# Kernel optimization log

Measured on AMD Instinct MI355X. Metric: run time of the kernel, lower is better.

## Reference

```python
import jax, jax.numpy as jnp
import numpy as np

D_MODEL = 1024
NUM_HEADS = 16
D_K = D_MODEL // NUM_HEADS


def setup_inputs() -> dict:
    key = jax.random.key(0)
    k1, k2, k3, k4 = jax.random.split(key, 4)
    scale = 1.0 / np.sqrt(D_MODEL)
    inp = {
        "input": jax.random.normal(k1, (2, 2048, D_MODEL), dtype=jnp.float32),
        "W_qkv": jax.random.normal(k2, (D_MODEL, 3 * D_MODEL), dtype=jnp.float32) * scale,
        "b_qkv": jax.random.normal(k3, (3 * D_MODEL,), dtype=jnp.float32) * 0.02,
        "W_out": jax.random.normal(k4, (D_MODEL, D_MODEL), dtype=jnp.float32) * scale,
    }
    return inp


def reference(input, W_qkv, b_qkv, W_out):
    B, S, _ = input.shape
    qkv = input @ W_qkv + b_qkv                      # [B,S,3D]
    q, k, v = jnp.split(qkv, 3, axis=-1)             # each [B,S,D]
    def heads(x):
        return x.reshape(B, S, NUM_HEADS, D_K).transpose(0, 2, 1, 3)  # [B,H,S,dk]
    q, k, v = heads(q), heads(k), heads(v)
    scores = jnp.einsum("bhsd,bhtd->bhst", q, k) / jnp.sqrt(jnp.float32(D_K))
    attn = jax.nn.softmax(scores, axis=-1)           # [B,H,S,S]
    out = jnp.einsum("bhst,bhtd->bhsd", attn, v)     # [B,H,S,dk]
    out = out.transpose(0, 2, 1, 3).reshape(B, S, D_MODEL)
    return out @ W_out
```

## Files before the change

### kernel.cpp

```cpp
#include <hip/hip_runtime.h>

typedef unsigned short u16;
typedef unsigned int u32;
typedef __attribute__((ext_vector_type(8))) short short8;
typedef __attribute__((ext_vector_type(8))) __bf16 bf16x8;
typedef __attribute__((ext_vector_type(4))) float f32x4;
typedef __attribute__((ext_vector_type(16))) float f32x16;

__device__ __forceinline__ u16 f2bf(float f) {
  union { float f; u32 u; } c; c.f = f;
  u32 u = c.u + 0x7fffu + ((c.u >> 16) & 1u);
  return (u16)(u >> 16);
}
__device__ __forceinline__ f32x4 mfma16(short8 a, short8 b, f32x4 c) {
  return __builtin_amdgcn_mfma_f32_16x16x32_bf16(
      __builtin_bit_cast(bf16x8, a), __builtin_bit_cast(bf16x8, b), c, 0, 0, 0);
}
__device__ __forceinline__ f32x16 mfma32(short8 a, short8 b, f32x16 c) {
  return __builtin_amdgcn_mfma_f32_32x32x16_bf16(
      __builtin_bit_cast(bf16x8, a), __builtin_bit_cast(bf16x8, b), c, 0, 0, 0);
}
__device__ __forceinline__ float fexp2(float x) {
  float r; asm("v_exp_f32 %0, %1" : "=v"(r) : "v"(x)); return r;
}
__device__ __forceinline__ void gl16(const u16* g, u16* l) {
  __builtin_amdgcn_global_load_lds(
      (const __attribute__((address_space(1))) unsigned*)g,
      (__attribute__((address_space(3))) unsigned*)l, 16, 0, 0);
}


__global__ __launch_bounds__(256) void transpose_f32_bf16(const float* __restrict__ in,
                                                          u16* __restrict__ out,
                                                          int R, int C) {
  __shared__ u16 tile[32][33];
  int tx = threadIdx.x & 31, ty = threadIdx.x >> 5;
  int c0 = blockIdx.x * 32, r0 = blockIdx.y * 32;
  for (int i = 0; i < 32; i += 8)
    tile[ty + i][tx] = f2bf(in[(size_t)(r0 + ty + i) * C + c0 + tx]);
  __syncthreads();
  for (int i = 0; i < 32; i += 8)
    out[(size_t)(c0 + ty + i) * R + r0 + tx] = tile[tx][ty + i];
}

template <int MODE, int BM>
__global__ __launch_bounds__(256) void gemm_bt(const void* __restrict__ Av,
                                               const void* __restrict__ Bv,
                                               const float* __restrict__ bias,
                                               void* __restrict__ C0v,
                                               void* __restrict__ C1v,
                                               int M, int N, int K) {
  constexpr int MI  = BM / 32;
  constexpr int NSA = BM / 8;
  constexpr int ASZ = (MODE == 1) ? 9216 : NSA * 512;
  constexpr int BSZ = (MODE == 2) ? 9216 : 8192;
  __shared__ __align__(16) u16 As[2][ASZ];
  __shared__ __align__(16) u16 Bs[2][BSZ];
  const int tid = threadIdx.x;
  const int w = tid >> 6, l = tid & 63;
  const int i16 = l & 15, q4 = l >> 4;

  const int nbx = gridDim.x;
  const int nwg = nbx * gridDim.y;
  int fid = blockIdx.y * nbx + blockIdx.x;
  int wg = (nwg & 7) ? fid : ((fid & 7) * (nwg >> 3) + (fid >> 3));
  const int m0 = (wg / nbx) * BM, n0 = (wg % nbx) * 128;
  const int wm = (w >> 1) * (BM / 2), wn = (w & 1) * 64;

  const int arow = tid >> 3, akg = (tid & 7) * 8;

  const u16* A16p = (const u16*)Av;
  const u16* B16p = (const u16*)Bv;
  const float* Fp = (MODE == 1) ? (const float*)Av : (const float*)Bv;
  const int fbase = (MODE == 1) ? m0 : n0;

  f32x4 acc[MI][4] = {};
  float4 pf[4][2];

#define STAGE_A16(bufi, kk) {                                                  \
    _Pragma("unroll") for (int i = 0; i < NSA / 4; ++i) {                      \
      const int s = w * (NSA / 4) + i;                                         \
      gl16(&A16p[(size_t)(m0 + (s >> 1) * 16 + i16) * K + (kk) + (s & 1) * 32  \
                 + q4 * 8],                                                    \
           &As[bufi][s * 512]); } }
#define STAGE_B16(bufi, kk) {                                                  \
    _Pragma("unroll") for (int i = 0; i < 4; ++i) {                            \
      const int s = w * 4 + i;                                                 \
      gl16(&B16p[(size_t)(n0 + (s >> 1) * 16 + i16) * K + (kk) + (s & 1) * 32  \
                 + q4 * 8],                                                    \
           &Bs[bufi][s * 512]); } }
#define LOAD_PFX(kk) {                                                         \
    _Pragma("unroll") for (int i = 0; i < 4; ++i) {                            \
      const float* src = Fp + (size_t)(fbase + arow + i * 32) * K + (kk) + akg;\
      pf[i][0] = *(const float4*)src;                                          \
      pf[i][1] = *(const float4*)(src + 4); } }
#define CVT_X(bufi) {                                                          \
    _Pragma("unroll") for (int i = 0; i < 4; ++i) {                            \
      short8 v;                                                                \
      v[0] = (short)f2bf(pf[i][0].x); v[1] = (short)f2bf(pf[i][0].y);          \
      v[2] = (short)f2bf(pf[i][0].z); v[3] = (short)f2bf(pf[i][0].w);          \
      v[4] = (short)f2bf(pf[i][1].x); v[5] = (short)f2bf(pf[i][1].y);          \
      v[6] = (short)f2bf(pf[i][1].z); v[7] = (short)f2bf(pf[i][1].w);          \
      u16* d = (MODE == 1) ? &As[bufi][(arow + i * 32) * 72 + akg]             \
                           : &Bs[bufi][(arow + i * 32) * 72 + akg];            \
      *(short8*)d = v; } }

  const int nk = K >> 6;
  if constexpr (MODE == 0) {
    STAGE_A16(0, 0); STAGE_B16(0, 0);
  } else if constexpr (MODE == 1) {
    LOAD_PFX(0); STAGE_B16(0, 0); CVT_X(0); LOAD_PFX(64);
  } else {
    LOAD_PFX(0); STAGE_A16(0, 0); CVT_X(0); LOAD_PFX(64);
  }
  __syncthreads();

  for (int t = 0; t < nk; ++t) {
    const int cur = t & 1, nxt = cur ^ 1;
    const int k1 = (t + 1) << 6;
    if (t + 1 < nk) {
      if constexpr (MODE == 0) {
        STAGE_A16(nxt, k1); STAGE_B16(nxt, k1);
      } else if constexpr (MODE == 1) {
        STAGE_B16(nxt, k1); CVT_X(nxt);
        if (t + 2 < nk) LOAD_PFX(k1 + 64);
      } else {
        STAGE_A16(nxt, k1); CVT_X(nxt);
        if (t + 2 < nk) LOAD_PFX(k1 + 64);
      }
    }
#pragma unroll
    for (int ks = 0; ks < 2; ++ks) {
      short8 af[MI], bfr[4];
#pragma unroll
      for (int mi = 0; mi < MI; ++mi) {
        if constexpr (MODE == 1)
          af[mi] = *(short8*)&As[cur][(wm + mi * 16 + i16) * 72 + ks * 32 + q4 * 8];
        else
          af[mi] = *(short8*)((char*)&As[cur][0] +
                              (((wm >> 4) + mi) * 2 + ks) * 1024 + l * 16);
      }
#pragma unroll
      for (int ni = 0; ni < 4; ++ni) {
        if constexpr (MODE == 2)
          bfr[ni] = *(short8*)&Bs[cur][(wn + ni * 16 + i16) * 72 + ks * 32 + q4 * 8];
        else
          bfr[ni] = *(short8*)((char*)&Bs[cur][0] +
                               (((wn >> 4) + ni) * 2 + ks) * 1024 + l * 16);
      }
#pragma unroll
      for (int mi = 0; mi < MI; ++mi)
#pragma unroll
        for (int ni = 0; ni < 4; ++ni)
          acc[mi][ni] = mfma16(af[mi], bfr[ni], acc[mi][ni]);
    }
    __syncthreads();
  }
#undef STAGE_A16
#undef STAGE_B16
#undef LOAD_PFX
#undef CVT_X

  if constexpr (MODE == 0) {
    float* dstf = (float*)C0v;
    for (int mi = 0; mi < MI; ++mi) {
      int row = m0 + wm + mi * 16 + q4 * 4;
      for (int ni = 0; ni < 4; ++ni) {
        int nl = wn + ni * 16 + i16;
        for (int r = 0; r < 4; ++r)
          dstf[(size_t)(row + r) * N + n0 + nl] = acc[mi][ni][r];
      }
    }
  } else if constexpr (MODE == 1) {
    if (n0 < 1024) {
      u16* dstb = (u16*)C0v;
      for (int mi = 0; mi < MI; ++mi) {
        int row = m0 + wm + mi * 16 + q4 * 4;
        for (int ni = 0; ni < 4; ++ni) {
          int nl = wn + ni * 16 + i16;
          float b = bias[n0 + nl];
          for (int r = 0; r < 4; ++r)
            dstb[(size_t)(row + r) * 1024 + n0 + nl] = f2bf(acc[mi][ni][r] + b);
        }
      }
    } else {
      u16* KT = (u16*)C1v;
      for (int mi = 0; mi < MI; ++mi) {
        int row = m0 + wm + mi * 16 + q4 * 4;
        for (int ni = 0; ni < 4; ++ni) {
          int nl = wn + ni * 16 + i16;
          const int d = (n0 - 1024) + nl;
          const int hh = d >> 6, dh = d & 63;
          const int sd = (dh >> 4) << 1;
          const int lh = ((dh >> 3) & 1) << 5;
          const int j = dh & 7;
          float b = bias[n0 + nl];
          for (int r = 0; r < 4; ++r) {
            const int tok = row + r;
            const int bb = tok >> 11, t = tok & 2047;
            size_t addr = ((size_t)((bb << 4) + hh) * 32 + (t >> 6)) * 4096
                        + (sd + ((t >> 5) & 1)) * 512 + (lh + (t & 31)) * 8 + j;
            KT[addr] = f2bf(acc[mi][ni][r] + b);
          }
        }
      }
    }
  } else {
    u16* VTt = (u16*)C0v;
    for (int mi = 0; mi < MI; ++mi) {
      int drow = m0 + wm + mi * 16 + q4 * 4;
      float4 bv = *(const float4*)&bias[drow];
      const float bvr[4] = {bv.x, bv.y, bv.z, bv.w};
      for (int ni = 0; ni < 4; ++ni) {
        int col = n0 + wn + ni * 16 + i16;
        const int bb = col >> 11, t = col & 2047;
        const int su = ((t >> 4) & 3) << 1;
        const int lt = ((t >> 3) & 1) << 5;
        const int j = t & 7;
        const size_t tb0 = ((size_t)(bb << 4) * 32 + (t >> 6)) * 4096;
        for (int r = 0; r < 4; ++r) {
          const int d = drow + r;
          const int hh = d >> 6, dh = d & 63;
          size_t addr = tb0 + (size_t)hh * 131072
                      + (su + (dh >> 5)) * 512 + (lt + (dh & 31)) * 8 + j;
          VTt[addr] = f2bf(acc[mi][ni][r] + bvr[r]);
        }
      }
    }
  }
}

__global__ __launch_bounds__(512, 4) void attn_flash(u16* __restrict__ Qbuf,
                                                     const u16* __restrict__ Kall,
                                                     const u16* __restrict__ VTall) {
  constexpr float CSC = 0.18033688011112042f;
  constexpr float MC  = 96.0f * CSC;
  __shared__ __align__(16) u16 SH[32768];
  __shared__ float RsumB[128], RsumT[128];

  const int tid = threadIdx.x;
  const int w = tid >> 6, l = tid & 63;
  const int l31 = l & 31, hi = l >> 5;
  const int qg = w >> 1, th = w & 1;

  u16* KsL = SH + th * 16384;
  u16* VsL = SH + th * 16384 + 8192;

  const int L = blockIdx.x;
  const int xcd = L & 7, rr = L >> 3;
  const int qb = rr & 15, gg = rr >> 4;
  const int g = gg * 8 + xcd;
  const int h = g & 15, bat = g >> 4;
  const int q0 = qb * 128;

  u16* Q = Qbuf + (size_t)bat * 2048 * 1024;
  const u16* ksrc = Kall + (size_t)((bat << 4) + h) * 131072 + l * 8;
  const u16* vsrc = VTall + (size_t)((bat << 4) + h) * 131072 + l * 8;

  short8 qf[4];
  {
    const u16* qrow = Q + (size_t)(q0 + qg * 32 + l31) * 1024 + h * 64 + hi * 8;
#pragma unroll
    for (int ks = 0; ks < 4; ++ks) qf[ks] = *(const short8*)(qrow + ks * 16);
  }

#define STAGE(buf_, it_) {                                                   \
    const size_t toff = (size_t)(it_) * 4096;                                \
    gl16(ksrc + toff + qg * 512,       KsL + (buf_) * 4096 + qg * 512);      \
    gl16(ksrc + toff + (qg + 4) * 512, KsL + (buf_) * 4096 + (qg + 4) * 512);\
    gl16(vsrc + toff + qg * 512,       VsL + (buf_) * 4096 + qg * 512);      \
    gl16(vsrc + toff + (qg + 4) * 512, VsL + (buf_) * 4096 + (qg + 4) * 512); }

  f32x16 o0 = {}, o1 = {};
  float sm0 = 0.f, sm1 = 0.f, sm2 = 0.f, sm3 = 0.f;

  const int tbase = th * 16;
  STAGE(0, tbase);
  __syncthreads();

  for (int i = 0; i < 16; ++i) {
    const int cur = i & 1;
    if (i + 1 < 16) STAGE(cur ^ 1, tbase + i + 1);

    const char* Kc = (const char*)KsL + cur * 8192 + l * 16;
    const char* Vc = (const char*)VsL + cur * 8192 + l * 16;

    f32x16 st0 = {}, st1 = {};
#pragma unroll
    for (int ks = 0; ks < 4; ++ks) {
      short8 kf0 = *(const short8*)(Kc + ks * 2048);
      short8 kf1 = *(const short8*)(Kc + ks * 2048 + 1024);
      st0 = mfma32(kf0, qf[ks], st0);
      st1 = mfma32(kf1, qf[ks], st1);
    }

    u32 W[16];
#define SOFTMAX_PACK(stt, WB) {                                             \
      float p_[16];                                                         \
      _Pragma("unroll") for (int r = 0; r < 16; ++r)                        \
          p_[r] = fexp2(__builtin_fmaf(stt[r], CSC, -MC));                  \
      _Pragma("unroll") for (int r = 0; r < 16; r += 4) {                   \
        sm0 += p_[r]; sm1 += p_[r + 1]; sm2 += p_[r + 2]; sm3 += p_[r + 3]; \
      }                                                                     \
      _Pragma("unroll") for (int m = 0; m < 4; ++m)                         \
        _Pragma("unroll") for (int s = 0; s < 2; ++s)                       \
          asm("v_cvt_pk_bf16_f32 %0, %1, %2"                                \
              : "=v"(W[(WB) + m * 2 + s])                                   \
              : "v"(p_[4 * m + 2 * s]), "v"(p_[4 * m + 2 * s + 1]));        \
    }
    SOFTMAX_PACK(st0, 0)
    SOFTMAX_PACK(st1, 8)
#undef SOFTMAX_PACK

#pragma unroll
    for (int u = 0; u < 4; ++u) {
      const int base = (u >> 1) * 8 + (u & 1) * 4;
      u32 a0 = W[base], a1 = W[base + 1], b0 = W[base + 2], b1 = W[base + 3];
      asm("v_permlane32_swap_b32 %0, %1" : "+v"(a0), "+v"(b0));
      asm("v_permlane32_swap_b32 %0, %1" : "+v"(a1), "+v"(b1));
      int4 af4;
      af4.x = (int)a0; af4.y = (int)a1; af4.z = (int)b0; af4.w = (int)b1;
      const short8 pfr = __builtin_bit_cast(short8, af4);
      const short8 vf0 = *(const short8*)(Vc + u * 2048);
      const short8 vf1 = *(const short8*)(Vc + u * 2048 + 1024);
      o0 = mfma32(pfr, vf0, o0);
      o1 = mfma32(pfr, vf1, o1);
    }
    __syncthreads();
  }
#undef STAGE

  float rs = (sm0 + sm1) + (sm2 + sm3);
  rs += __shfl_xor(rs, 32);
  __syncthreads();
  float* MF = (float*)SH;
  if (th == 1) {
    float* dst = MF + (qg * 64 + l) * 36;
    *(f32x16*)dst = o0;
    *(f32x16*)(dst + 16) = o1;
    if (hi == 0) RsumB[qg * 32 + l31] = rs;
  }
  __syncthreads();
  if (th == 0) {
    const float* src = MF + (qg * 64 + l) * 36;
    o0 += *(const f32x16*)src;
    o1 += *(const f32x16*)(src + 16);
    float rtot = rs + RsumB[qg * 32 + l31];
    if (hi == 0) RsumT[qg * 32 + l31] = rtot;
  }
  __syncthreads();
  if (th == 0) {
#pragma unroll
    for (int r = 0; r < 16; ++r) {
      const int qq = (r & 3) + 8 * (r >> 2) + 4 * hi;
      const float inv = 1.0f / RsumT[qg * 32 + qq];
      u16* dst = Q + (size_t)(q0 + qg * 32 + qq) * 1024 + h * 64 + l31;
      dst[0]  = f2bf(o0[r] * inv);
      dst[32] = f2bf(o1[r] * inv);
    }
  }
}

extern "C" void kernel_launch(void* const* d_in, const int* in_sizes, int n_in,
                              void* d_out, int out_size, void* d_ws, size_t ws_size,
                              hipStream_t stream) {
  const float* X    = (const float*)d_in[0];
  const float* Wqkv = (const float*)d_in[1];
  const float* bqkv = (const float*)d_in[2];
  const float* Wout = (const float*)d_in[3];

  u16* Qbuf = (u16*)d_out;
  u16* WT1  = Qbuf + (size_t)4096 * 1024;
  u16* WT2  = WT1 + (size_t)3072 * 1024;
  u16* Kbuf = (u16*)d_ws;
  u16* VT   = Kbuf + (size_t)4096 * 1024;
  float* Cws = (float*)d_ws;

  transpose_f32_bf16<<<dim3(96, 32), 256, 0, stream>>>(Wqkv, WT1, 1024, 3072);
  transpose_f32_bf16<<<dim3(32, 32), 256, 0, stream>>>(Wout, WT2, 1024, 1024);

  gemm_bt<1, 128><<<dim3(16, 32), 256, 0, stream>>>(
      X, WT1, bqkv, Qbuf, Kbuf, 4096, 2048, 1024);

  gemm_bt<2, 64><<<dim3(32, 16), 256, 0, stream>>>(
      WT1 + (size_t)2048 * 1024, X, bqkv + 2048, VT, nullptr, 1024, 4096, 1024);

  attn_flash<<<dim3(512), 512, 0, stream>>>(Qbuf, Kbuf, VT);

  gemm_bt<0, 64><<<dim3(8, 64), 256, 0, stream>>>(
      Qbuf, WT2, nullptr, Cws, nullptr, 4096, 1024, 1024);

  hipMemcpyAsync(d_out, Cws, (size_t)4096 * 1024 * sizeof(float),
                 hipMemcpyDeviceToDevice, stream);
}
```

Before: 218.8 us.

## Pre-convert X to bf16, retile QK projection GEMM, add MFMA priority hints

Adds a standalone kernel that converts the fp32 input X to bf16 once. The Q/K projection GEMM can then stage both operands with direct global-to-LDS bf16 loads instead of converting fp32 in registers, and it is retiled from BM=128 to BM=64 with twice as many workgroups. The attention kernel wraps its two MFMA phases in s_setprio raises so the matrix work gets issue priority over the softmax phase of other waves. The workspace is reorganized so the bf16 X buffer is later overwritten by V^T. The cost is an extra launch plus an extra pass over X in memory.

```diff
diff --git a/kernel.cpp b/kernel.cpp
--- a/kernel.cpp
+++ b/kernel.cpp
@@ -41,6 +41,19 @@
   __syncthreads();
   for (int i = 0; i < 32; i += 8)
     out[(size_t)(c0 + ty + i) * R + r0 + tx] = tile[tx][ty + i];
+}
+
+__global__ __launch_bounds__(256) void f32_to_bf16(const float* __restrict__ in,
+                                                   u16* __restrict__ out) {
+  const size_t base = ((size_t)blockIdx.x * 256 + threadIdx.x) * 8;
+  float4 f0 = *(const float4*)(in + base);
+  float4 f1 = *(const float4*)(in + base + 4);
+  short8 v;
+  v[0] = (short)f2bf(f0.x); v[1] = (short)f2bf(f0.y);
+  v[2] = (short)f2bf(f0.z); v[3] = (short)f2bf(f0.w);
+  v[4] = (short)f2bf(f1.x); v[5] = (short)f2bf(f1.y);
+  v[6] = (short)f2bf(f1.z); v[7] = (short)f2bf(f1.w);
+  *(short8*)&out[base] = v;
 }
 
 template <int MODE, int BM>
@@ -52,7 +65,7 @@
                                                int M, int N, int K) {
   constexpr int MI  = BM / 32;
   constexpr int NSA = BM / 8;
-  constexpr int ASZ = (MODE == 1) ? 9216 : NSA * 512;
+  constexpr int ASZ = NSA * 512;
   constexpr int BSZ = (MODE == 2) ? 9216 : 8192;
   __shared__ __align__(16) u16 As[2][ASZ];
   __shared__ __align__(16) u16 Bs[2][BSZ];
@@ -71,8 +84,8 @@
 
   const u16* A16p = (const u16*)Av;
   const u16* B16p = (const u16*)Bv;
-  const float* Fp = (MODE == 1) ? (const float*)Av : (const float*)Bv;
-  const int fbase = (MODE == 1) ? m0 : n0;
+  const float* Fp = (const float*)Bv;
+  const int fbase = n0;
 
   f32x4 acc[MI][4] = {};
   float4 pf[4][2];
@@ -101,17 +114,13 @@
       v[2] = (short)f2bf(pf[i][0].z); v[3] = (short)f2bf(pf[i][0].w);          \
       v[4] = (short)f2bf(pf[i][1].x); v[5] = (short)f2bf(pf[i][1].y);          \
       v[6] = (short)f2bf(pf[i][1].z); v[7] = (short)f2bf(pf[i][1].w);          \
-      u16* d = (MODE == 1) ? &As[bufi][(arow + i * 32) * 72 + akg]             \
-                           : &Bs[bufi][(arow + i * 32) * 72 + akg];            \
-      *(short8*)d = v; } }
+      *(short8*)&Bs[bufi][(arow + i * 32) * 72 + akg] = v; } }
 
   const int nk = K >> 6;
-  if constexpr (MODE == 0) {
+  if constexpr (MODE == 2) {
+    LOAD_PFX(0); STAGE_A16(0, 0); CVT_X(0); LOAD_PFX(64);
+  } else {
     STAGE_A16(0, 0); STAGE_B16(0, 0);
-  } else if constexpr (MODE == 1) {
-    LOAD_PFX(0); STAGE_B16(0, 0); CVT_X(0); LOAD_PFX(64);
-  } else {
-    LOAD_PFX(0); STAGE_A16(0, 0); CVT_X(0); LOAD_PFX(64);
   }
   __syncthreads();
 
@@ -119,27 +128,20 @@
     const int cur = t & 1, nxt = cur ^ 1;
     const int k1 = (t + 1) << 6;
     if (t + 1 < nk) {
-      if constexpr (MODE == 0) {
-        STAGE_A16(nxt, k1); STAGE_B16(nxt, k1);
-      } else if constexpr (MODE == 1) {
-        STAGE_B16(nxt, k1); CVT_X(nxt);
+      if constexpr (MODE == 2) {
+        STAGE_A16(nxt, k1); CVT_X(nxt);
         if (t + 2 < nk) LOAD_PFX(k1 + 64);
       } else {
-        STAGE_A16(nxt, k1); CVT_X(nxt);
-        if (t + 2 < nk) LOAD_PFX(k1 + 64);
+        STAGE_A16(nxt, k1); STAGE_B16(nxt, k1);
       }
     }
 #pragma unroll
     for (int ks = 0; ks < 2; ++ks) {
       short8 af[MI], bfr[4];
 #pragma unroll
-      for (int mi = 0; mi < MI; ++mi) {
-        if constexpr (MODE == 1)
-          af[mi] = *(short8*)&As[cur][(wm + mi * 16 + i16) * 72 + ks * 32 + q4 * 8];
-        else
-          af[mi] = *(short8*)((char*)&As[cur][0] +
-                              (((wm >> 4) + mi) * 2 + ks) * 1024 + l * 16);
-      }
+      for (int mi = 0; mi < MI; ++mi)
+        af[mi] = *(short8*)((char*)&As[cur][0] +
+                            (((wm >> 4) + mi) * 2 + ks) * 1024 + l * 16);
 #pragma unroll
       for (int ni = 0; ni < 4; ++ni) {
         if constexpr (MODE == 2)
@@ -286,6 +288,7 @@
     const char* Vc = (const char*)VsL + cur * 8192 + l * 16;
 
     f32x16 st0 = {}, st1 = {};
+    __builtin_amdgcn_s_setprio(1);
 #pragma unroll
     for (int ks = 0; ks < 4; ++ks) {
       short8 kf0 = *(const short8*)(Kc + ks * 2048);
@@ -293,6 +296,7 @@
       st0 = mfma32(kf0, qf[ks], st0);
       st1 = mfma32(kf1, qf[ks], st1);
     }
+    __builtin_amdgcn_s_setprio(0);
 
     u32 W[16];
 #define SOFTMAX_PACK(stt, WB) {                                             \
@@ -312,6 +316,7 @@
     SOFTMAX_PACK(st1, 8)
 #undef SOFTMAX_PACK
 
+    __builtin_amdgcn_s_setprio(1);
 #pragma unroll
     for (int u = 0; u < 4; ++u) {
       const int base = (u >> 1) * 8 + (u & 1) * 4;
@@ -326,6 +331,7 @@
       o0 = mfma32(pfr, vf0, o0);
       o1 = mfma32(pfr, vf1, o1);
     }
+    __builtin_amdgcn_s_setprio(0);
     __syncthreads();
   }
 #undef STAGE
@@ -372,20 +378,22 @@
   u16* Qbuf = (u16*)d_out;
   u16* WT1  = Qbuf + (size_t)4096 * 1024;
   u16* WT2  = WT1 + (size_t)3072 * 1024;
-  u16* Kbuf = (u16*)d_ws;
-  u16* VT   = Kbuf + (size_t)4096 * 1024;
+  u16* Xbf  = (u16*)d_ws;
+  u16* Kt   = (u16*)d_ws + (size_t)4096 * 1024;
+  u16* VTt  = (u16*)d_ws;
   float* Cws = (float*)d_ws;
 
   transpose_f32_bf16<<<dim3(96, 32), 256, 0, stream>>>(Wqkv, WT1, 1024, 3072);
   transpose_f32_bf16<<<dim3(32, 32), 256, 0, stream>>>(Wout, WT2, 1024, 1024);
-
-  gemm_bt<1, 128><<<dim3(16, 32), 256, 0, stream>>>(
-      X, WT1, bqkv, Qbuf, Kbuf, 4096, 2048, 1024);
+  f32_to_bf16<<<dim3(2048), 256, 0, stream>>>(X, Xbf);
+
+  gemm_bt<1, 64><<<dim3(16, 64), 256, 0, stream>>>(
+      Xbf, WT1, bqkv, Qbuf, Kt, 4096, 2048, 1024);
 
   gemm_bt<2, 64><<<dim3(32, 16), 256, 0, stream>>>(
-      WT1 + (size_t)2048 * 1024, X, bqkv + 2048, VT, nullptr, 1024, 4096, 1024);
-
-  attn_flash<<<dim3(512), 512, 0, stream>>>(Qbuf, Kbuf, VT);
+      WT1 + (size_t)2048 * 1024, X, bqkv + 2048, VTt, nullptr, 1024, 4096, 1024);
+
+  attn_flash<<<dim3(512), 512, 0, stream>>>(Qbuf, Kt, VTt);
 
   gemm_bt<0, 64><<<dim3(8, 64), 256, 0, stream>>>(
       Qbuf, WT2, nullptr, Cws, nullptr, 4096, 1024, 1024);
```

After: 245.1 us. 1.12x slower.

## Fuse Q/K/V projections into one GEMM with MFMA-tiled Q and output layout

Applied to the files above, without the earlier changes.

Merges the separate QKV GEMM (Q,K) and transposed V GEMM into a single launch over N=3072, with the V epilogue scattering into the tiled V layout directly. Q and the attention output are stored in a pre-swizzled 64x64 tile layout, so attention and the output-projection GEMM can load fragments contiguously (gl16 of whole tiles). This also removes the second pass that re-read and re-converted X to bf16. Adds s_setprio around MFMA blocks in attention. The epilogue scatter stores become more irregular, which may cost write efficiency.

```diff
diff --git a/kernel.cpp b/kernel.cpp
--- a/kernel.cpp
+++ b/kernel.cpp
@@ -45,17 +45,17 @@
 
 template <int MODE, int BM>
 __global__ __launch_bounds__(256) void gemm_bt(const void* __restrict__ Av,
-                                               const void* __restrict__ Bv,
+                                               const u16* __restrict__ Bv,
                                                const float* __restrict__ bias,
                                                void* __restrict__ C0v,
                                                void* __restrict__ C1v,
+                                               void* __restrict__ C2v,
                                                int M, int N, int K) {
   constexpr int MI  = BM / 32;
   constexpr int NSA = BM / 8;
   constexpr int ASZ = (MODE == 1) ? 9216 : NSA * 512;
-  constexpr int BSZ = (MODE == 2) ? 9216 : 8192;
   __shared__ __align__(16) u16 As[2][ASZ];
-  __shared__ __align__(16) u16 Bs[2][BSZ];
+  __shared__ __align__(16) u16 Bs[2][8192];
   const int tid = threadIdx.x;
   const int w = tid >> 6, l = tid & 63;
   const int i16 = l & 15, q4 = l >> 4;
@@ -70,28 +70,25 @@
   const int arow = tid >> 3, akg = (tid & 7) * 8;
 
   const u16* A16p = (const u16*)Av;
-  const u16* B16p = (const u16*)Bv;
-  const float* Fp = (MODE == 1) ? (const float*)Av : (const float*)Bv;
-  const int fbase = (MODE == 1) ? m0 : n0;
-
+  const float* Fp = (const float*)Av;
   f32x4 acc[MI][4] = {};
   float4 pf[4][2];
 
 #define STAGE_A16(bufi, kk) {                                                  \
     _Pragma("unroll") for (int i = 0; i < NSA / 4; ++i) {                      \
       const int s = w * (NSA / 4) + i;                                         \
-      gl16(&A16p[(size_t)(m0 + (s >> 1) * 16 + i16) * K + (kk) + (s & 1) * 32  \
-                 + q4 * 8],                                                    \
+      gl16(&A16p[((size_t)((m0 >> 6) * 16 + ((kk) >> 6))) * 4096 + s * 512     \
+                 + l * 8],                                                     \
            &As[bufi][s * 512]); } }
 #define STAGE_B16(bufi, kk) {                                                  \
     _Pragma("unroll") for (int i = 0; i < 4; ++i) {                            \
       const int s = w * 4 + i;                                                 \
-      gl16(&B16p[(size_t)(n0 + (s >> 1) * 16 + i16) * K + (kk) + (s & 1) * 32  \
-                 + q4 * 8],                                                    \
+      gl16(&Bv[(size_t)(n0 + (s >> 1) * 16 + i16) * K + (kk) + (s & 1) * 32    \
+               + q4 * 8],                                                      \
            &Bs[bufi][s * 512]); } }
 #define LOAD_PFX(kk) {                                                         \
     _Pragma("unroll") for (int i = 0; i < 4; ++i) {                            \
-      const float* src = Fp + (size_t)(fbase + arow + i * 32) * K + (kk) + akg;\
+      const float* src = Fp + (size_t)(m0 + arow + i * 32) * K + (kk) + akg;   \
       pf[i][0] = *(const float4*)src;                                          \
       pf[i][1] = *(const float4*)(src + 4); } }
 #define CVT_X(bufi) {                                                          \
@@ -101,17 +98,13 @@
       v[2] = (short)f2bf(pf[i][0].z); v[3] = (short)f2bf(pf[i][0].w);          \
       v[4] = (short)f2bf(pf[i][1].x); v[5] = (short)f2bf(pf[i][1].y);          \
       v[6] = (short)f2bf(pf[i][1].z); v[7] = (short)f2bf(pf[i][1].w);          \
-      u16* d = (MODE == 1) ? &As[bufi][(arow + i * 32) * 72 + akg]             \
-                           : &Bs[bufi][(arow + i * 32) * 72 + akg];            \
-      *(short8*)d = v; } }
+      *(short8*)&As[bufi][(arow + i * 32) * 72 + akg] = v; } }
 
   const int nk = K >> 6;
-  if constexpr (MODE == 0) {
-    STAGE_A16(0, 0); STAGE_B16(0, 0);
-  } else if constexpr (MODE == 1) {
+  if constexpr (MODE == 1) {
     LOAD_PFX(0); STAGE_B16(0, 0); CVT_X(0); LOAD_PFX(64);
   } else {
-    LOAD_PFX(0); STAGE_A16(0, 0); CVT_X(0); LOAD_PFX(64);
+    STAGE_A16(0, 0); STAGE_B16(0, 0);
   }
   __syncthreads();
 
@@ -119,14 +112,11 @@
     const int cur = t & 1, nxt = cur ^ 1;
     const int k1 = (t + 1) << 6;
     if (t + 1 < nk) {
-      if constexpr (MODE == 0) {
-        STAGE_A16(nxt, k1); STAGE_B16(nxt, k1);
-      } else if constexpr (MODE == 1) {
+      if constexpr (MODE == 1) {
         STAGE_B16(nxt, k1); CVT_X(nxt);
         if (t + 2 < nk) LOAD_PFX(k1 + 64);
       } else {
-        STAGE_A16(nxt, k1); CVT_X(nxt);
-        if (t + 2 < nk) LOAD_PFX(k1 + 64);
+        STAGE_A16(nxt, k1); STAGE_B16(nxt, k1);
       }
     }
 #pragma unroll
@@ -141,13 +131,9 @@
                               (((wm >> 4) + mi) * 2 + ks) * 1024 + l * 16);
       }
 #pragma unroll
-      for (int ni = 0; ni < 4; ++ni) {
-        if constexpr (MODE == 2)
-          bfr[ni] = *(short8*)&Bs[cur][(wn + ni * 16 + i16) * 72 + ks * 32 + q4 * 8];
-        else
-          bfr[ni] = *(short8*)((char*)&Bs[cur][0] +
-                               (((wn >> 4) + ni) * 2 + ks) * 1024 + l * 16);
-      }
+      for (int ni = 0; ni < 4; ++ni)
+        bfr[ni] = *(short8*)((char*)&Bs[cur][0] +
+                             (((wn >> 4) + ni) * 2 + ks) * 1024 + l * 16);
 #pragma unroll
       for (int mi = 0; mi < MI; ++mi)
 #pragma unroll
@@ -171,30 +157,31 @@
           dstf[(size_t)(row + r) * N + n0 + nl] = acc[mi][ni][r];
       }
     }
-  } else if constexpr (MODE == 1) {
-    if (n0 < 1024) {
-      u16* dstb = (u16*)C0v;
-      for (int mi = 0; mi < MI; ++mi) {
-        int row = m0 + wm + mi * 16 + q4 * 4;
-        for (int ni = 0; ni < 4; ++ni) {
-          int nl = wn + ni * 16 + i16;
-          float b = bias[n0 + nl];
-          for (int r = 0; r < 4; ++r)
-            dstb[(size_t)(row + r) * 1024 + n0 + nl] = f2bf(acc[mi][ni][r] + b);
-        }
-      }
-    } else {
-      u16* KT = (u16*)C1v;
-      for (int mi = 0; mi < MI; ++mi) {
-        int row = m0 + wm + mi * 16 + q4 * 4;
-        for (int ni = 0; ni < 4; ++ni) {
-          int nl = wn + ni * 16 + i16;
+  } else {
+    for (int mi = 0; mi < MI; ++mi) {
+      int row = m0 + wm + mi * 16 + q4 * 4;
+      for (int ni = 0; ni < 4; ++ni) {
+        int nl = wn + ni * 16 + i16;
+        float b = bias[n0 + nl];
+        if (n0 < 1024) {
+          u16* Qt = (u16*)C0v;
+          const int d = n0 + nl;
+          const int dt = d >> 6, dh = d & 63;
+          const int sc = (dh >> 5), sl = (((dh & 31) >> 3) << 4), j = dh & 7;
+          for (int r = 0; r < 4; ++r) {
+            const int tok = row + r;
+            size_t addr = ((size_t)((tok >> 6) * 16 + dt)) * 4096
+                        + ((((tok & 63) >> 4) << 1) + sc) * 512
+                        + ((tok & 15) + sl) * 8 + j;
+            Qt[addr] = f2bf(acc[mi][ni][r] + b);
+          }
+        } else if (n0 < 2048) {
+          u16* KT = (u16*)C1v;
           const int d = (n0 - 1024) + nl;
           const int hh = d >> 6, dh = d & 63;
           const int sd = (dh >> 4) << 1;
           const int lh = ((dh >> 3) & 1) << 5;
           const int j = dh & 7;
-          float b = bias[n0 + nl];
           for (int r = 0; r < 4; ++r) {
             const int tok = row + r;
             const int bb = tok >> 11, t = tok & 2047;
@@ -202,28 +189,18 @@
                         + (sd + ((t >> 5) & 1)) * 512 + (lh + (t & 31)) * 8 + j;
             KT[addr] = f2bf(acc[mi][ni][r] + b);
           }
-        }
-      }
-    }
-  } else {
-    u16* VTt = (u16*)C0v;
-    for (int mi = 0; mi < MI; ++mi) {
-      int drow = m0 + wm + mi * 16 + q4 * 4;
-      float4 bv = *(const float4*)&bias[drow];
-      const float bvr[4] = {bv.x, bv.y, bv.z, bv.w};
-      for (int ni = 0; ni < 4; ++ni) {
-        int col = n0 + wn + ni * 16 + i16;
-        const int bb = col >> 11, t = col & 2047;
-        const int su = ((t >> 4) & 3) << 1;
-        const int lt = ((t >> 3) & 1) << 5;
-        const int j = t & 7;
-        const size_t tb0 = ((size_t)(bb << 4) * 32 + (t >> 6)) * 4096;
-        for (int r = 0; r < 4; ++r) {
-          const int d = drow + r;
+        } else {
+          u16* VTt = (u16*)C2v;
+          const int d = (n0 - 2048) + nl;
           const int hh = d >> 6, dh = d & 63;
-          size_t addr = tb0 + (size_t)hh * 131072
-                      + (su + (dh >> 5)) * 512 + (lt + (dh & 31)) * 8 + j;
-          VTt[addr] = f2bf(acc[mi][ni][r] + bvr[r]);
+          for (int r = 0; r < 4; ++r) {
+            const int tok = row + r;
+            const int bb = tok >> 11, t = tok & 2047;
+            size_t addr = ((size_t)((bb << 4) + hh) * 32 + (t >> 6)) * 4096
+                        + ((((t & 63) >> 4) << 1) + (dh >> 5)) * 512
+                        + ((((t >> 3) & 1) << 5) + (dh & 31)) * 8 + (t & 7);
+            VTt[addr] = f2bf(acc[mi][ni][r] + b);
+          }
         }
       }
     }
@@ -259,9 +236,15 @@
 
   short8 qf[4];
   {
-    const u16* qrow = Q + (size_t)(q0 + qg * 32 + l31) * 1024 + h * 64 + hi * 8;
-#pragma unroll
-    for (int ks = 0; ks < 4; ++ks) qf[ks] = *(const short8*)(qrow + ks * 16);
+    const int mt = (q0 >> 6) + (qg >> 1);
+    const u16* qtile = Q + ((size_t)mt * 16 + h) * 4096;
+    const int rg = (qg & 1) * 2 + (l31 >> 4);
+#pragma unroll
+    for (int ks = 0; ks < 4; ++ks) {
+      const int s = rg * 2 + (ks >> 1);
+      const int slot = (l31 & 15) + ((((ks & 1) << 1) + hi) << 4);
+      qf[ks] = *(const short8*)(qtile + s * 512 + slot * 8);
+    }
   }
 
 #define STAGE(buf_, it_) {                                                   \
@@ -286,6 +269,7 @@
     const char* Vc = (const char*)VsL + cur * 8192 + l * 16;
 
     f32x16 st0 = {}, st1 = {};
+    __builtin_amdgcn_s_setprio(1);
 #pragma unroll
     for (int ks = 0; ks < 4; ++ks) {
       short8 kf0 = *(const short8*)(Kc + ks * 2048);
@@ -293,6 +277,7 @@
       st0 = mfma32(kf0, qf[ks], st0);
       st1 = mfma32(kf1, qf[ks], st1);
     }
+    __builtin_amdgcn_s_setprio(0);
 
     u32 W[16];
 #define SOFTMAX_PACK(stt, WB) {                                             \
@@ -312,6 +297,7 @@
     SOFTMAX_PACK(st1, 8)
 #undef SOFTMAX_PACK
 
+    __builtin_amdgcn_s_setprio(1);
 #pragma unroll
     for (int u = 0; u < 4; ++u) {
       const int base = (u >> 1) * 8 + (u & 1) * 4;
@@ -326,6 +312,7 @@
       o0 = mfma32(pfr, vf0, o0);
       o1 = mfma32(pfr, vf1, o1);
     }
+    __builtin_amdgcn_s_setprio(0);
     __syncthreads();
   }
 #undef STAGE
@@ -354,9 +341,12 @@
     for (int r = 0; r < 16; ++r) {
       const int qq = (r & 3) + 8 * (r >> 2) + 4 * hi;
       const float inv = 1.0f / RsumT[qg * 32 + qq];
-      u16* dst = Q + (size_t)(q0 + qg * 32 + qq) * 1024 + h * 64 + l31;
-      dst[0]  = f2bf(o0[r] * inv);
-      dst[32] = f2bf(o1[r] * inv);
+      const int tok = q0 + qg * 32 + qq;
+      u16* ot = Q + ((size_t)(tok >> 6) * 16 + h) * 4096;
+      const int sbase = (((tok & 63) >> 4) << 1);
+      const int slot = ((tok & 15) + ((l31 >> 3) << 4)) * 8 + (l31 & 7);
+      ot[sbase * 512 + slot]         = f2bf(o0[r] * inv);
+      ot[(sbase + 1) * 512 + slot]   = f2bf(o1[r] * inv);
     }
   }
 }
@@ -369,26 +359,23 @@
   const float* bqkv = (const float*)d_in[2];
   const float* Wout = (const float*)d_in[3];
 
-  u16* Qbuf = (u16*)d_out;
-  u16* WT1  = Qbuf + (size_t)4096 * 1024;
+  u16* Qt   = (u16*)d_out;
+  u16* WT1  = Qt + (size_t)4096 * 1024;
   u16* WT2  = WT1 + (size_t)3072 * 1024;
-  u16* Kbuf = (u16*)d_ws;
-  u16* VT   = Kbuf + (size_t)4096 * 1024;
+  u16* VTt  = (u16*)d_ws;
+  u16* Kt   = (u16*)d_ws + (size_t)4096 * 1024;
   float* Cws = (float*)d_ws;
 
   transpose_f32_bf16<<<dim3(96, 32), 256, 0, stream>>>(Wqkv, WT1, 1024, 3072);
   transpose_f32_bf16<<<dim3(32, 32), 256, 0, stream>>>(Wout, WT2, 1024, 1024);
 
-  gemm_bt<1, 128><<<dim3(16, 32), 256, 0, stream>>>(
-      X, WT1, bqkv, Qbuf, Kbuf, 4096, 2048, 1024);
-
-  gemm_bt<2, 64><<<dim3(32, 16), 256, 0, stream>>>(
-      WT1 + (size_t)2048 * 1024, X, bqkv + 2048, VT, nullptr, 1024, 4096, 1024);
-
-  attn_flash<<<dim3(512), 512, 0, stream>>>(Qbuf, Kbuf, VT);
+  gemm_bt<1, 128><<<dim3(24, 32), 256, 0, stream>>>(
+      X, WT1, bqkv, Qt, Kt, VTt, 4096, 3072, 1024);
+
+  attn_flash<<<dim3(512), 512, 0, stream>>>(Qt, Kt, VTt);
 
   gemm_bt<0, 64><<<dim3(8, 64), 256, 0, stream>>>(
-      Qbuf, WT2, nullptr, Cws, nullptr, 4096, 1024, 1024);
+      Qt, WT2, nullptr, Cws, nullptr, nullptr, 4096, 1024, 1024);
 
   hipMemcpyAsync(d_out, Cws, (size_t)4096 * 1024 * sizeof(float),
                  hipMemcpyDeviceToDevice, stream);
```

Result: faster. 213.7 us (-2.3%).
